# Performance work log

Measured on AMD Instinct MI355X. Metric: run time of the kernel, lower is better.

## Reference

```python
import jax, jax.numpy as jnp
import numpy as np

M_SQRT1_2 = 0.7071067811865476
P_DROP = 0.1  # activation_dropout


def setup_inputs() -> dict:
    key = jax.random.key(0)
    k1, k2, k3, k4 = jax.random.split(key, 4)
    N, FFN, EMB = 8192, 4096, 1024
    x = jax.random.normal(k1, (N, FFN), dtype=jnp.float16)
    weight = (jax.random.normal(k2, (EMB, FFN), dtype=jnp.float32) * (1.0 / np.sqrt(FFN))).astype(jnp.float16)
    bias = jax.random.normal(k3, (EMB,), dtype=jnp.float16)
    mask = jax.random.uniform(k4, (N, FFN)) >= P_DROP  # keep mask (bool)
    return {"x": x, "weight": weight, "bias": bias, "mask": mask}


def reference(x, weight, bias, mask):
    # GELU computed in fp32, cast back to fp16 (matches the custom IR)
    xf = x.astype(jnp.float32)
    g = (0.5 * xf * (1.0 + jax.lax.erf(xf * M_SQRT1_2))).astype(jnp.float16)
    # dropout: mask then scale by 1/(1-p) in fp16
    scale = jnp.float16(1.0 / (1.0 - P_DROP))
    h = g * mask.astype(jnp.float16) * scale  # [N, FFN]
    # y[N0, N2] = sum_N1 h[N0, N1] * weight[N2, N1] + bias[N2]
    y = jnp.einsum('nf,ef->ne', h, weight) + bias[None, :]
    return y
```

## Files before the change

### kernel.cpp

```cpp
#include <hip/hip_runtime.h>
#include <stdint.h>

typedef uint32_t u32;
typedef uint16_t u16;

static constexpr int M_DIM = 8192;
static constexpr int N_DIM = 1024;
static constexpr int K_DIM = 4096;
static constexpr int BM = 128;
static constexpr int BN = 128;
static constexpr int BK = 32;
static constexpr int K_TILES = K_DIM / BK;
static constexpr int MB_TILES = M_DIM / 16;
static constexpr int NB_TILES = N_DIM / 16;

static constexpr size_t FRAG_U16 = 512;
static constexpr size_t HT_BYTES = (size_t)MB_TILES * K_TILES * FRAG_U16 * 2;
static constexpr size_t WT_BYTES = (size_t)NB_TILES * K_TILES * FRAG_U16 * 2;
static constexpr size_t WS_NEEDED = HT_BYTES + WT_BYTES;

typedef __attribute__((ext_vector_type(8))) _Float16 half8;
typedef __attribute__((ext_vector_type(4))) float f32x4;

__device__ __forceinline__ u32 pack2(float a, float b) {
  union { _Float16 h[2]; u32 u; } p;
  p.h[0] = (_Float16)a;
  p.h[1] = (_Float16)b;
  return p.u;
}

__device__ __forceinline__ float gelu_drop(float x, u32 keep) {
  float ax = fabsf(x);
  float z  = ax * 0.70710678f;
  float t  = __builtin_amdgcn_rcpf(fmaf(0.3275911f, z, 1.0f));
  float poly = fmaf(fmaf(fmaf(fmaf(1.061405429f, t, -1.453152027f),
                              t, 1.421413741f),
                         t, -0.284496736f),
                    t, 0.254829592f) * t;
  float e   = exp2f(z * z * -1.44269504f);
  float erf = fmaf(-poly, e, 1.0f);
  float g   = 0.5f * x * (1.0f + copysignf(erf, x));
  return keep ? g * 1.1111112f : 0.0f;
}

__device__ __forceinline__ void async_cp16(const void* g, void* l) {
  __builtin_amdgcn_global_load_lds((__attribute__((address_space(1))) u32*)g,
                                   (__attribute__((address_space(3))) u32*)l,
                                   16, 0, 0);
}

static constexpr int H_WAVES = MB_TILES * K_TILES;
static constexpr int W_WAVES = NB_TILES * K_TILES;
static constexpr int PACK_BLOCKS = (H_WAVES + W_WAVES) / 4;

__global__ __launch_bounds__(256)
void pack_kernel(const float* __restrict__ X, const int* __restrict__ Mask,
                 const float* __restrict__ W, u16* __restrict__ Ht, u16* __restrict__ Wt) {
  const int l     = threadIdx.x & 63;
  const int fi    = blockIdx.x * 4 + (threadIdx.x >> 6);
  const int row16 = l & 15;
  const int kof   = (l >> 4) << 3;

  if (fi < H_WAVES) {
    const int mb = fi >> 7, kt = fi & 127;
    const float* xp = X    + (size_t)(mb * 16 + row16) * K_DIM + kt * 32 + kof;
    const int*   mp = Mask + (size_t)(mb * 16 + row16) * K_DIM + kt * 32 + kof;
    float4 x0 = *(const float4*)(xp + 0);
    float4 x1 = *(const float4*)(xp + 4);
    uint4  m0 = *(const uint4*)(mp + 0);
    uint4  m1 = *(const uint4*)(mp + 4);
    u32 o0 = pack2(gelu_drop(x0.x, m0.x), gelu_drop(x0.y, m0.y));
    u32 o1 = pack2(gelu_drop(x0.z, m0.z), gelu_drop(x0.w, m0.w));
    u32 o2 = pack2(gelu_drop(x1.x, m1.x), gelu_drop(x1.y, m1.y));
    u32 o3 = pack2(gelu_drop(x1.z, m1.z), gelu_drop(x1.w, m1.w));
    *(uint4*)(Ht + (size_t)fi * FRAG_U16 + l * 8) = make_uint4(o0, o1, o2, o3);
  } else {
    const int fj = fi - H_WAVES;
    const int nb = fj >> 7, kt = fj & 127;
    const float* wp = W + (size_t)(nb * 16 + row16) * K_DIM + kt * 32 + kof;
    float4 w0 = *(const float4*)(wp + 0);
    float4 w1 = *(const float4*)(wp + 4);
    u32 o0 = pack2(w0.x, w0.y);
    u32 o1 = pack2(w0.z, w0.w);
    u32 o2 = pack2(w1.x, w1.y);
    u32 o3 = pack2(w1.z, w1.w);
    *(uint4*)(Wt + (size_t)fj * FRAG_U16 + l * 8) = make_uint4(o0, o1, o2, o3);
  }
}

__global__ __launch_bounds__(256, 2)
void gemm_kernel(const u16* __restrict__ Ht, const u16* __restrict__ Wt,
                 const float* __restrict__ Bias, float* __restrict__ Out) {
  __shared__ __attribute__((aligned(16))) u16 Abuf[2][BM * BK];
  __shared__ __attribute__((aligned(16))) u16 Bbuf[2][BN * BK];

  const int tid  = threadIdx.x;
  const int lane = tid & 63;
  const int wv   = tid >> 6;
  const int wr   = wv >> 1;
  const int wc   = wv & 1;

  const int bm = blockIdx.x & 63;
  const int bn = blockIdx.x >> 6;
  const int m0 = bm * BM;
  const int n0 = bn * BN;

  const char* aG = (const char*)Ht;
  const char* bG = (const char*)Wt;
  const size_t aOff0 = ((size_t)(bm * 8 +     (tid >> 6)) * K_TILES) * 1024 + (size_t)lane * 16;
  const size_t aOff1 = ((size_t)(bm * 8 + 4 + (tid >> 6)) * K_TILES) * 1024 + (size_t)lane * 16;
  const size_t bOff0 = ((size_t)(bn * 8 +     (tid >> 6)) * K_TILES) * 1024 + (size_t)lane * 16;
  const size_t bOff1 = ((size_t)(bn * 8 + 4 + (tid >> 6)) * K_TILES) * 1024 + (size_t)lane * 16;

  f32x4 acc[4][4];
#pragma unroll
  for (int i = 0; i < 4; ++i)
#pragma unroll
    for (int j = 0; j < 4; ++j)
      acc[i][j] = (f32x4){0.f, 0.f, 0.f, 0.f};

  {
    async_cp16(aG + aOff0, (char*)Abuf[0] + tid * 16);
    async_cp16(aG + aOff1, (char*)Abuf[0] + (tid + 256) * 16);
    async_cp16(bG + bOff0, (char*)Bbuf[0] + tid * 16);
    async_cp16(bG + bOff1, (char*)Bbuf[0] + (tid + 256) * 16);
  }
  __syncthreads();

#pragma unroll 1
  for (int kt = 0; kt < K_TILES; ++kt) {
    const int cur = kt & 1;
    if (kt + 1 < K_TILES) {
      const size_t ko = (size_t)(kt + 1) * 1024;
      char* ad = (char*)Abuf[cur ^ 1];
      char* bd = (char*)Bbuf[cur ^ 1];
      async_cp16(aG + aOff0 + ko, ad + tid * 16);
      async_cp16(aG + aOff1 + ko, ad + (tid + 256) * 16);
      async_cp16(bG + bOff0 + ko, bd + tid * 16);
      async_cp16(bG + bOff1 + ko, bd + (tid + 256) * 16);
    }

    half8 ar[4], br[4];
#pragma unroll
    for (int i = 0; i < 4; ++i)
      ar[i] = *(const half8*)((const char*)Abuf[cur] + ((wr * 4 + i) * 64 + lane) * 16);
#pragma unroll
    for (int j = 0; j < 4; ++j)
      br[j] = *(const half8*)((const char*)Bbuf[cur] + ((wc * 4 + j) * 64 + lane) * 16);

#pragma unroll
    for (int i = 0; i < 4; ++i)
#pragma unroll
      for (int j = 0; j < 4; ++j)
        acc[i][j] = __builtin_amdgcn_mfma_f32_16x16x32_f16(ar[i], br[j], acc[i][j], 0, 0, 0);

    __syncthreads();
  }

  const int fr = lane & 15;
  const int rq = (lane >> 4) << 2;
  float bv[4];
#pragma unroll
  for (int j = 0; j < 4; ++j)
    bv[j] = Bias[n0 + wc * 64 + j * 16 + fr];

#pragma unroll
  for (int i = 0; i < 4; ++i) {
    const int row0 = m0 + wr * 64 + i * 16 + rq;
#pragma unroll
    for (int j = 0; j < 4; ++j) {
      const int col = n0 + wc * 64 + j * 16 + fr;
#pragma unroll
      for (int r = 0; r < 4; ++r) {
        Out[(size_t)(row0 + r) * N_DIM + col] = acc[i][j][r] + bv[j];
      }
    }
  }
}

static constexpr int A_STRIDE = 40;

__global__ __launch_bounds__(256, 2)
void fused_fallback_kernel(const float* __restrict__ X, const float* __restrict__ W,
                           const float* __restrict__ Bias, const int* __restrict__ Mask,
                           float* __restrict__ Out) {
  __shared__ __attribute__((aligned(16))) _Float16 As[BM * A_STRIDE];
  __shared__ __attribute__((aligned(16))) _Float16 Bs[BN * BK];

  const int tid  = threadIdx.x;
  const int lane = tid & 63;
  const int wv   = tid >> 6;
  const int wr   = wv >> 1;
  const int wc   = wv & 1;
  const int bm = blockIdx.x & 63;
  const int bn = blockIdx.x >> 6;
  const int m0 = bm * BM;
  const int n0 = bn * BN;

  const int a_m = tid >> 1;
  const int a_k = (tid & 1) << 4;
  const float* xptr = X    + (size_t)(m0 + a_m) * K_DIM + a_k;
  const int*   mptr = Mask + (size_t)(m0 + a_m) * K_DIM + a_k;
  _Float16* a_lds = &As[a_m * A_STRIDE + a_k];

  const int i0 = tid, i1 = tid + 256;
  const float* wp0 = W + (size_t)(n0 + (i0 >> 2)) * K_DIM + ((i0 & 3) << 3);
  const float* wp1 = W + (size_t)(n0 + (i1 >> 2)) * K_DIM + ((i1 & 3) << 3);
  _Float16* bl0 = &Bs[i0 * 8];
  _Float16* bl1 = &Bs[i1 * 8];

  f32x4 acc[4][4];
#pragma unroll
  for (int i = 0; i < 4; ++i)
#pragma unroll
    for (int j = 0; j < 4; ++j)
      acc[i][j] = (f32x4){0.f, 0.f, 0.f, 0.f};

  float4 xf0 = *(const float4*)(xptr +  0);
  float4 xf1 = *(const float4*)(xptr +  4);
  float4 xf2 = *(const float4*)(xptr +  8);
  float4 xf3 = *(const float4*)(xptr + 12);
  uint4  mr0 = *(const uint4*)(mptr +  0);
  uint4  mr1 = *(const uint4*)(mptr +  4);
  uint4  mr2 = *(const uint4*)(mptr +  8);
  uint4  mr3 = *(const uint4*)(mptr + 12);
  float4 wf0 = *(const float4*)(wp0 + 0);
  float4 wf1 = *(const float4*)(wp0 + 4);
  float4 wf2 = *(const float4*)(wp1 + 0);
  float4 wf3 = *(const float4*)(wp1 + 4);

#pragma unroll 1
  for (int kt = 0; kt < K_TILES; ++kt) {
    {
      float xs[16] = {xf0.x, xf0.y, xf0.z, xf0.w, xf1.x, xf1.y, xf1.z, xf1.w,
                      xf2.x, xf2.y, xf2.z, xf2.w, xf3.x, xf3.y, xf3.z, xf3.w};
      u32 mk[16]   = {mr0.x, mr0.y, mr0.z, mr0.w, mr1.x, mr1.y, mr1.z, mr1.w,
                      mr2.x, mr2.y, mr2.z, mr2.w, mr3.x, mr3.y, mr3.z, mr3.w};
      u32 ow[8];
#pragma unroll
      for (int e = 0; e < 8; ++e)
        ow[e] = pack2(gelu_drop(xs[2 * e], mk[2 * e]), gelu_drop(xs[2 * e + 1], mk[2 * e + 1]));
      ((uint4*)a_lds)[0] = make_uint4(ow[0], ow[1], ow[2], ow[3]);
      ((uint4*)a_lds)[1] = make_uint4(ow[4], ow[5], ow[6], ow[7]);
    }
    {
      *(uint4*)bl0 = make_uint4(pack2(wf0.x, wf0.y), pack2(wf0.z, wf0.w),
                                pack2(wf1.x, wf1.y), pack2(wf1.z, wf1.w));
      *(uint4*)bl1 = make_uint4(pack2(wf2.x, wf2.y), pack2(wf2.z, wf2.w),
                                pack2(wf3.x, wf3.y), pack2(wf3.z, wf3.w));
    }
    __syncthreads();

    if (kt + 1 < K_TILES) {
      xptr += BK; mptr += BK; wp0 += BK; wp1 += BK;
      xf0 = *(const float4*)(xptr +  0);
      xf1 = *(const float4*)(xptr +  4);
      xf2 = *(const float4*)(xptr +  8);
      xf3 = *(const float4*)(xptr + 12);
      mr0 = *(const uint4*)(mptr +  0);
      mr1 = *(const uint4*)(mptr +  4);
      mr2 = *(const uint4*)(mptr +  8);
      mr3 = *(const uint4*)(mptr + 12);
      wf0 = *(const float4*)(wp0 + 0);
      wf1 = *(const float4*)(wp0 + 4);
      wf2 = *(const float4*)(wp1 + 0);
      wf3 = *(const float4*)(wp1 + 4);
    }

    {
      const int fr2 = lane & 15;
      const int fk2 = (lane >> 4) << 3;
      half8 ar[4], br[4];
#pragma unroll
      for (int i = 0; i < 4; ++i)
        ar[i] = *(const half8*)&As[(wr * 64 + i * 16 + fr2) * A_STRIDE + fk2];
#pragma unroll
      for (int j = 0; j < 4; ++j)
        br[j] = *(const half8*)&Bs[(wc * 64 + j * 16 + fr2) * BK + fk2];
#pragma unroll
      for (int i = 0; i < 4; ++i)
#pragma unroll
        for (int j = 0; j < 4; ++j)
          acc[i][j] = __builtin_amdgcn_mfma_f32_16x16x32_f16(ar[i], br[j], acc[i][j], 0, 0, 0);
    }
    __syncthreads();
  }

  const int fr = lane & 15;
  const int rq = (lane >> 4) << 2;
  float bv[4];
#pragma unroll
  for (int j = 0; j < 4; ++j)
    bv[j] = Bias[n0 + wc * 64 + j * 16 + fr];
#pragma unroll
  for (int i = 0; i < 4; ++i) {
    const int row0 = m0 + wr * 64 + i * 16 + rq;
#pragma unroll
    for (int j = 0; j < 4; ++j) {
      const int col = n0 + wc * 64 + j * 16 + fr;
#pragma unroll
      for (int r = 0; r < 4; ++r)
        Out[(size_t)(row0 + r) * N_DIM + col] = acc[i][j][r] + bv[j];
    }
  }
}

extern "C" void kernel_launch(void* const* d_in, const int* in_sizes, int n_in,
                              void* d_out, int out_size, void* d_ws, size_t ws_size,
                              hipStream_t stream) {
  const float* X    = (const float*)d_in[0];
  const float* W    = (const float*)d_in[1];
  const float* Bias = (const float*)d_in[2];
  const int*   Mk   = (const int*)d_in[3];
  float* Out = (float*)d_out;

  if (ws_size >= WS_NEEDED) {
    u16* Ht = (u16*)d_ws;
    u16* Wt = (u16*)((char*)d_ws + HT_BYTES);
    pack_kernel<<<PACK_BLOCKS, 256, 0, stream>>>(X, Mk, W, Ht, Wt);
    gemm_kernel<<<(M_DIM / BM) * (N_DIM / BN), 256, 0, stream>>>(Ht, Wt, Bias, Out);
  } else {
    fused_fallback_kernel<<<(M_DIM / BM) * (N_DIM / BN), 256, 0, stream>>>(X, W, Bias, Mk, Out);
  }
}
```

Baseline: 415.7 us.

## Widen GEMM tile to 128x256x64 with B fragments loaded directly into registers

The GEMM kernel moves to 512 threads (8 waves in a 2x4 grid) with a 128x256 output tile and a K step of 64. A tiles still go through double-buffered LDS via async global-to-LDS copies. Each wave now loads its own W fragments straight from global memory into registers, using a ping-pong pair of register sets, so the B shared buffer is removed. The aim is to halve the number of K-loop barriers, improve reuse of A per load, and take the B LDS traffic off the critical path. The cost is higher register pressure and exposed global-load latency on B, and the grid shrinks to 256 blocks, which may underfill the GPU.

```diff
diff --git a/kernel.cpp b/kernel.cpp
--- a/kernel.cpp
+++ b/kernel.cpp
@@ -7,20 +7,24 @@
 static constexpr int M_DIM = 8192;
 static constexpr int N_DIM = 1024;
 static constexpr int K_DIM = 4096;
+
 static constexpr int BM = 128;
-static constexpr int BN = 128;
-static constexpr int BK = 32;
-static constexpr int K_TILES = K_DIM / BK;
+static constexpr int BN = 256;
+static constexpr int BK = 64;
+static constexpr int KT64 = K_DIM / BK;
+static constexpr int K_TILES32 = K_DIM / 32;
 static constexpr int MB_TILES = M_DIM / 16;
 static constexpr int NB_TILES = N_DIM / 16;
 
 static constexpr size_t FRAG_U16 = 512;
-static constexpr size_t HT_BYTES = (size_t)MB_TILES * K_TILES * FRAG_U16 * 2;
-static constexpr size_t WT_BYTES = (size_t)NB_TILES * K_TILES * FRAG_U16 * 2;
+static constexpr size_t HT_BYTES = (size_t)MB_TILES * K_TILES32 * FRAG_U16 * 2;
+static constexpr size_t WT_BYTES = (size_t)NB_TILES * K_TILES32 * FRAG_U16 * 2;
 static constexpr size_t WS_NEEDED = HT_BYTES + WT_BYTES;
 
 typedef __attribute__((ext_vector_type(8))) _Float16 half8;
 typedef __attribute__((ext_vector_type(4))) float f32x4;
+
+union u4h8 { uint4 u; half8 h; };
 
 __device__ __forceinline__ u32 pack2(float a, float b) {
   union { _Float16 h[2]; u32 u; } p;
@@ -49,8 +53,8 @@
                                    16, 0, 0);
 }
 
-static constexpr int H_WAVES = MB_TILES * K_TILES;
-static constexpr int W_WAVES = NB_TILES * K_TILES;
+static constexpr int H_WAVES = MB_TILES * K_TILES32;
+static constexpr int W_WAVES = NB_TILES * K_TILES32;
 static constexpr int PACK_BLOCKS = (H_WAVES + W_WAVES) / 4;
 
 __global__ __launch_bounds__(256)
@@ -80,25 +84,21 @@
     const float* wp = W + (size_t)(nb * 16 + row16) * K_DIM + kt * 32 + kof;
     float4 w0 = *(const float4*)(wp + 0);
     float4 w1 = *(const float4*)(wp + 4);
-    u32 o0 = pack2(w0.x, w0.y);
-    u32 o1 = pack2(w0.z, w0.w);
-    u32 o2 = pack2(w1.x, w1.y);
-    u32 o3 = pack2(w1.z, w1.w);
-    *(uint4*)(Wt + (size_t)fj * FRAG_U16 + l * 8) = make_uint4(o0, o1, o2, o3);
-  }
-}
-
-__global__ __launch_bounds__(256, 2)
+    *(uint4*)(Wt + (size_t)fj * FRAG_U16 + l * 8) =
+        make_uint4(pack2(w0.x, w0.y), pack2(w0.z, w0.w), pack2(w1.x, w1.y), pack2(w1.z, w1.w));
+  }
+}
+
+__global__ __launch_bounds__(512, 2)
 void gemm_kernel(const u16* __restrict__ Ht, const u16* __restrict__ Wt,
                  const float* __restrict__ Bias, float* __restrict__ Out) {
   __shared__ __attribute__((aligned(16))) u16 Abuf[2][BM * BK];
-  __shared__ __attribute__((aligned(16))) u16 Bbuf[2][BN * BK];
 
   const int tid  = threadIdx.x;
   const int lane = tid & 63;
   const int wv   = tid >> 6;
-  const int wr   = wv >> 1;
-  const int wc   = wv & 1;
+  const int wr   = wv >> 2;
+  const int wc   = wv & 3;
 
   const int bm = blockIdx.x & 63;
   const int bn = blockIdx.x >> 6;
@@ -106,11 +106,20 @@
   const int n0 = bn * BN;
 
   const char* aG = (const char*)Ht;
-  const char* bG = (const char*)Wt;
-  const size_t aOff0 = ((size_t)(bm * 8 +     (tid >> 6)) * K_TILES) * 1024 + (size_t)lane * 16;
-  const size_t aOff1 = ((size_t)(bm * 8 + 4 + (tid >> 6)) * K_TILES) * 1024 + (size_t)lane * 16;
-  const size_t bOff0 = ((size_t)(bn * 8 +     (tid >> 6)) * K_TILES) * 1024 + (size_t)lane * 16;
-  const size_t bOff1 = ((size_t)(bn * 8 + 4 + (tid >> 6)) * K_TILES) * 1024 + (size_t)lane * 16;
+  const int f2_0 = tid >> 6;
+  const int f2_1 = (tid + 512) >> 6;
+  const size_t aBase0 = ((size_t)(bm * 8 + (f2_0 >> 1)) * K_TILES32 + (f2_0 & 1)) * 1024 + (size_t)lane * 16;
+  const size_t aBase1 = ((size_t)(bm * 8 + (f2_1 >> 1)) * K_TILES32 + (f2_1 & 1)) * 1024 + (size_t)lane * 16;
+  char* aDst0[2] = {(char*)Abuf[0] + tid * 16, (char*)Abuf[1] + tid * 16};
+  char* aDst1[2] = {(char*)Abuf[0] + (tid + 512) * 16, (char*)Abuf[1] + (tid + 512) * 16};
+
+  const char* bp[8];
+#pragma unroll
+  for (int j = 0; j < 4; ++j)
+#pragma unroll
+    for (int kk = 0; kk < 2; ++kk)
+      bp[j * 2 + kk] = (const char*)Wt +
+          ((size_t)(bn * 16 + wc * 4 + j) * K_TILES32 + kk) * 1024 + (size_t)lane * 16;
 
   f32x4 acc[4][4];
 #pragma unroll
@@ -119,42 +128,61 @@
     for (int j = 0; j < 4; ++j)
       acc[i][j] = (f32x4){0.f, 0.f, 0.f, 0.f};
 
-  {
-    async_cp16(aG + aOff0, (char*)Abuf[0] + tid * 16);
-    async_cp16(aG + aOff1, (char*)Abuf[0] + (tid + 256) * 16);
-    async_cp16(bG + bOff0, (char*)Bbuf[0] + tid * 16);
-    async_cp16(bG + bOff1, (char*)Bbuf[0] + (tid + 256) * 16);
-  }
+  async_cp16(aG + aBase0, aDst0[0]);
+  async_cp16(aG + aBase1, aDst1[0]);
+  u4h8 brE[8], brO[8];
+#pragma unroll
+  for (int q = 0; q < 8; ++q) brE[q].u = *(const uint4*)(bp[q]);
   __syncthreads();
 
 #pragma unroll 1
-  for (int kt = 0; kt < K_TILES; ++kt) {
-    const int cur = kt & 1;
-    if (kt + 1 < K_TILES) {
-      const size_t ko = (size_t)(kt + 1) * 1024;
-      char* ad = (char*)Abuf[cur ^ 1];
-      char* bd = (char*)Bbuf[cur ^ 1];
-      async_cp16(aG + aOff0 + ko, ad + tid * 16);
-      async_cp16(aG + aOff1 + ko, ad + (tid + 256) * 16);
-      async_cp16(bG + bOff0 + ko, bd + tid * 16);
-      async_cp16(bG + bOff1 + ko, bd + (tid + 256) * 16);
-    }
-
-    half8 ar[4], br[4];
-#pragma unroll
-    for (int i = 0; i < 4; ++i)
-      ar[i] = *(const half8*)((const char*)Abuf[cur] + ((wr * 4 + i) * 64 + lane) * 16);
-#pragma unroll
-    for (int j = 0; j < 4; ++j)
-      br[j] = *(const half8*)((const char*)Bbuf[cur] + ((wc * 4 + j) * 64 + lane) * 16);
-
-#pragma unroll
-    for (int i = 0; i < 4; ++i)
-#pragma unroll
-      for (int j = 0; j < 4; ++j)
-        acc[i][j] = __builtin_amdgcn_mfma_f32_16x16x32_f16(ar[i], br[j], acc[i][j], 0, 0, 0);
-
-    __syncthreads();
+  for (int kt = 0; kt < KT64; kt += 2) {
+    {
+      const size_t ko = (size_t)(kt + 1) * 2048;
+      async_cp16(aG + aBase0 + ko, aDst0[1]);
+      async_cp16(aG + aBase1 + ko, aDst1[1]);
+#pragma unroll
+      for (int q = 0; q < 8; ++q) brO[q].u = *(const uint4*)(bp[q] + ko);
+
+      half8 ar[2][4];
+#pragma unroll
+      for (int kk = 0; kk < 2; ++kk)
+#pragma unroll
+        for (int i = 0; i < 4; ++i)
+          ar[kk][i] = *(const half8*)((const char*)Abuf[0] + (((wr * 4 + i) * 2 + kk) * 64 + lane) * 16);
+#pragma unroll
+      for (int kk = 0; kk < 2; ++kk)
+#pragma unroll
+        for (int i = 0; i < 4; ++i)
+#pragma unroll
+          for (int j = 0; j < 4; ++j)
+            acc[i][j] = __builtin_amdgcn_mfma_f32_16x16x32_f16(ar[kk][i], brE[j * 2 + kk].h, acc[i][j], 0, 0, 0);
+      __syncthreads();
+    }
+    {
+      if (kt + 2 < KT64) {
+        const size_t ko = (size_t)(kt + 2) * 2048;
+        async_cp16(aG + aBase0 + ko, aDst0[0]);
+        async_cp16(aG + aBase1 + ko, aDst1[0]);
+#pragma unroll
+        for (int q = 0; q < 8; ++q) brE[q].u = *(const uint4*)(bp[q] + ko);
+      }
+
+      half8 ar[2][4];
+#pragma unroll
+      for (int kk = 0; kk < 2; ++kk)
+#pragma unroll
+        for (int i = 0; i < 4; ++i)
+          ar[kk][i] = *(const half8*)((const char*)Abuf[1] + (((wr * 4 + i) * 2 + kk) * 64 + lane) * 16);
+#pragma unroll
+      for (int kk = 0; kk < 2; ++kk)
+#pragma unroll
+        for (int i = 0; i < 4; ++i)
+#pragma unroll
+          for (int j = 0; j < 4; ++j)
+            acc[i][j] = __builtin_amdgcn_mfma_f32_16x16x32_f16(ar[kk][i], brO[j * 2 + kk].h, acc[i][j], 0, 0, 0);
+      __syncthreads();
+    }
   }
 
   const int fr = lane & 15;
@@ -171,9 +199,8 @@
     for (int j = 0; j < 4; ++j) {
       const int col = n0 + wc * 64 + j * 16 + fr;
 #pragma unroll
-      for (int r = 0; r < 4; ++r) {
+      for (int r = 0; r < 4; ++r)
         Out[(size_t)(row0 + r) * N_DIM + col] = acc[i][j][r] + bv[j];
-      }
     }
   }
 }
@@ -184,8 +211,8 @@
 void fused_fallback_kernel(const float* __restrict__ X, const float* __restrict__ W,
                            const float* __restrict__ Bias, const int* __restrict__ Mask,
                            float* __restrict__ Out) {
-  __shared__ __attribute__((aligned(16))) _Float16 As[BM * A_STRIDE];
-  __shared__ __attribute__((aligned(16))) _Float16 Bs[BN * BK];
+  __shared__ __attribute__((aligned(16))) _Float16 As[128 * A_STRIDE];
+  __shared__ __attribute__((aligned(16))) _Float16 Bs[128 * 32];
 
   const int tid  = threadIdx.x;
   const int lane = tid & 63;
@@ -194,8 +221,8 @@
   const int wc   = wv & 1;
   const int bm = blockIdx.x & 63;
   const int bn = blockIdx.x >> 6;
-  const int m0 = bm * BM;
-  const int n0 = bn * BN;
+  const int m0 = bm * 128;
+  const int n0 = bn * 128;
 
   const int a_m = tid >> 1;
   const int a_k = (tid & 1) << 4;
@@ -230,7 +257,7 @@
   float4 wf3 = *(const float4*)(wp1 + 4);
 
 #pragma unroll 1
-  for (int kt = 0; kt < K_TILES; ++kt) {
+  for (int kt = 0; kt < 128; ++kt) {
     {
       float xs[16] = {xf0.x, xf0.y, xf0.z, xf0.w, xf1.x, xf1.y, xf1.z, xf1.w,
                       xf2.x, xf2.y, xf2.z, xf2.w, xf3.x, xf3.y, xf3.z, xf3.w};
@@ -251,8 +278,8 @@
     }
     __syncthreads();
 
-    if (kt + 1 < K_TILES) {
-      xptr += BK; mptr += BK; wp0 += BK; wp1 += BK;
+    if (kt + 1 < 128) {
+      xptr += 32; mptr += 32; wp0 += 32; wp1 += 32;
       xf0 = *(const float4*)(xptr +  0);
       xf1 = *(const float4*)(xptr +  4);
       xf2 = *(const float4*)(xptr +  8);
@@ -276,7 +303,7 @@
         ar[i] = *(const half8*)&As[(wr * 64 + i * 16 + fr2) * A_STRIDE + fk2];
 #pragma unroll
       for (int j = 0; j < 4; ++j)
-        br[j] = *(const half8*)&Bs[(wc * 64 + j * 16 + fr2) * BK + fk2];
+        br[j] = *(const half8*)&Bs[(wc * 64 + j * 16 + fr2) * 32 + fk2];
 #pragma unroll
       for (int i = 0; i < 4; ++i)
 #pragma unroll
@@ -318,8 +345,8 @@
     u16* Ht = (u16*)d_ws;
     u16* Wt = (u16*)((char*)d_ws + HT_BYTES);
     pack_kernel<<<PACK_BLOCKS, 256, 0, stream>>>(X, Mk, W, Ht, Wt);
-    gemm_kernel<<<(M_DIM / BM) * (N_DIM / BN), 256, 0, stream>>>(Ht, Wt, Bias, Out);
+    gemm_kernel<<<(M_DIM / BM) * (N_DIM / BN), 512, 0, stream>>>(Ht, Wt, Bias, Out);
   } else {
-    fused_fallback_kernel<<<(M_DIM / BM) * (N_DIM / BN), 256, 0, stream>>>(X, W, Bias, Mk, Out);
-  }
-}
+    fused_fallback_kernel<<<64 * 8, 256, 0, stream>>>(X, W, Bias, Mk, Out);
+  }
+}
```

Measured after the change: 397.3 us. 4.4% less time.
